# Kernel tuning notes

Measured on AMD Instinct MI355X. Metric: run time of the kernel, lower is better.

The kernel has to match this reference:

```python
import jax, jax.numpy as jnp
import numpy as np

BETA = 0.9
THR = 1.0
ALPHA = 2.0  # snntorch surrogate.atan default

@jax.custom_vjp
def atan_spike(x):
    return (x > 0).astype(x.dtype)

def _atan_fwd(x):
    return atan_spike(x), x

def _atan_bwd(x, g):
    # snntorch ATan surrogate: alpha/2 / (1 + (pi/2 * alpha * x)^2)
    return (g * (ALPHA / 2.0) / (1.0 + (jnp.pi / 2.0 * ALPHA * x) ** 2),)

atan_spike.defvjp(_atan_fwd, _atan_bwd)

def setup_inputs() -> dict:
    key = jax.random.key(0)
    k = jax.random.split(key, 5)
    B, T, C, H, W = 128, 25, 3, 64, 64
    F, HID, O = C * H * W, 2048, 2
    bound1 = 1.0 / np.sqrt(F)
    boundo = 1.0 / np.sqrt(HID)
    return {
        "x": jax.random.normal(k[0], (B, T, C, H, W), jnp.float32),
        "W1": jax.random.uniform(k[1], (HID, F), jnp.float32, -bound1, bound1),
        "b1": jax.random.uniform(k[2], (HID,), jnp.float32, -bound1, bound1),
        "Wo": jax.random.uniform(k[3], (O, HID), jnp.float32, -boundo, boundo),
        "bo": jax.random.uniform(k[4], (O,), jnp.float32, -boundo, boundo),
    }

def reference(x, W1, b1, Wo, bo):
    B, T = x.shape[0], x.shape[1]
    HID, O = W1.shape[0], Wo.shape[0]
    xf = x.reshape(B, T, -1).transpose(1, 0, 2)  # [T, B, F]
    # fc1 for all timesteps at once (input is fixed per step)
    h_all = jnp.einsum('tbf,hf->tbh', xf, W1) + b1  # [T, B, HID]

    def step(carry, h):
        mem1, memo = carry
        # snntorch Leaky (reset_mechanism='subtract'): reset from previous mem
        r1 = atan_spike(mem1 - THR)
        mem1 = BETA * mem1 + h - r1 * THR
        s1 = atan_spike(mem1 - THR)
        o = s1 @ Wo.T + bo
        ro = atan_spike(memo - THR)
        memo = BETA * memo + o - ro * THR
        so = atan_spike(memo - THR)
        return (mem1, memo), so

    init = (jnp.zeros((B, HID), x.dtype), jnp.zeros((B, O), x.dtype))
    (_, _), spk_rec = jax.lax.scan(step, init, h_all)
    # train=False path: sum of output spikes over time
    return spk_rec.sum(axis=0)  # [B, O]
```

## Files before the change

kernel.cpp:

```cpp
#include <hip/hip_runtime.h>


#define T_STEPS 25
#define B_SZ    128
#define F_SZ    12288
#define HID_SZ  2048
#define KSTEPS  384
#define CHUNK   16384

typedef __attribute__((ext_vector_type(8))) _Float16 f16x8;
typedef __attribute__((ext_vector_type(4))) float f32x4;

__device__ __forceinline__ void g2l16(const void* g, void* l) {
  __builtin_amdgcn_global_load_lds(
      (const __attribute__((address_space(1))) void*)g,
      (__attribute__((address_space(3))) void*)l, 16, 0, 0);
}

__global__ __launch_bounds__(256) void conv_x_kernel(
    const float* __restrict__ x, char* __restrict__ A2) {
  const int total = T_STEPS * KSTEPS * 128 * 4;
  for (int i = blockIdx.x * 256 + threadIdx.x; i < total; i += gridDim.x * 256) {
    const int s = i & 3;
    const int r = (i >> 2) & 127;
    const int rest = i >> 9;
    const int ks = rest % KSTEPS;
    const int t = rest / KSTEPS;
    const int k0 = ks * 32 + s * 8;
    const float* src = x + ((size_t)r * T_STEPS + t) * F_SZ + k0;
    float4 v0 = *(const float4*)src;
    float4 v1 = *(const float4*)(src + 4);
    float vf[8] = {v0.x, v0.y, v0.z, v0.w, v1.x, v1.y, v1.z, v1.w};
    f16x8 hi, lo;
#pragma unroll
    for (int j = 0; j < 8; ++j) {
      _Float16 h = (_Float16)vf[j];
      hi[j] = h;
      lo[j] = (_Float16)(vf[j] - (float)h);
    }
    char* chunk = A2 + (size_t)rest * CHUNK;
    const int p = s ^ (r & 7);
    *(f16x8*)(chunk + r * 128 + p * 16) = hi;
    *(f16x8*)(chunk + r * 128 + (p ^ 4) * 16) = lo;
  }
}

__global__ __launch_bounds__(256) void conv_w_kernel(
    const float* __restrict__ W1, char* __restrict__ B2) {
  const int total = 16 * KSTEPS * 128 * 4;
  for (int i = blockIdx.x * 256 + threadIdx.x; i < total; i += gridDim.x * 256) {
    const int s = i & 3;
    const int r = (i >> 2) & 127;
    const int rest = i >> 9;
    const int ks = rest % KSTEPS;
    const int nt = rest / KSTEPS;
    const int k0 = ks * 32 + s * 8;
    const float* src = W1 + ((size_t)(nt * 128 + r)) * F_SZ + k0;
    float4 v0 = *(const float4*)src;
    float4 v1 = *(const float4*)(src + 4);
    float vf[8] = {v0.x, v0.y, v0.z, v0.w, v1.x, v1.y, v1.z, v1.w};
    f16x8 hi, lo;
#pragma unroll
    for (int j = 0; j < 8; ++j) {
      float vs = vf[j] * 128.0f;
      _Float16 h = (_Float16)vs;
      hi[j] = h;
      lo[j] = (_Float16)(vs - (float)h);
    }
    char* chunk = B2 + (size_t)rest * CHUNK;
    const int p = s ^ (r & 7);
    *(f16x8*)(chunk + r * 128 + p * 16) = hi;
    *(f16x8*)(chunk + r * 128 + (p ^ 4) * 16) = lo;
  }
}

__global__ __launch_bounds__(256, 2) void gemm_split_kernel(
    const char* __restrict__ A2, const char* __restrict__ B2,
    const float* __restrict__ b1, float* __restrict__ h_all) {
  __shared__ __align__(16) char lds[32768];
  const int tid = threadIdx.x;
  const int l = tid & 63;
  const int w = tid >> 6;
  const int wm = w >> 1, wn = w & 1;

  const int bid = blockIdx.x;
  const int swz = (bid & 7) * 50 + (bid >> 3);
  const int mt = swz >> 4;
  const int nt = swz & 15;
  const char* aSrc = A2 + (size_t)mt * KSTEPS * CHUNK;
  const char* bSrc = B2 + (size_t)nt * KSTEPS * CHUNK;

  f32x4 acc[4][4];
#pragma unroll
  for (int i = 0; i < 4; ++i)
#pragma unroll
    for (int j = 0; j < 4; ++j) acc[i][j] = (f32x4){0.f, 0.f, 0.f, 0.f};

  const int ra = wm * 64 + (l & 15);
  const int rb = wn * 64 + (l & 15);
  const int j4 = l >> 4;

  for (int k = 0; k < KSTEPS; ++k) {
    const char* ga = aSrc + (size_t)k * CHUNK + tid * 16;
    const char* gb = bSrc + (size_t)k * CHUNK + tid * 16;
    char* la = lds + w * 1024;
    char* lb = lds + 16384 + w * 1024;
#pragma unroll
    for (int i = 0; i < 4; ++i) g2l16(ga + i * 4096, la + i * 4096);
#pragma unroll
    for (int i = 0; i < 4; ++i) g2l16(gb + i * 4096, lb + i * 4096);
    __syncthreads();

    f16x8 ah[4], al[4], bh[4], bl[4];
#pragma unroll
    for (int mb = 0; mb < 4; ++mb) {
      const int r = ra + mb * 16;
      const char* base = lds + r * 128;
      ah[mb] = *(const f16x8*)(base + ((j4 ^ (r & 7)) << 4));
      al[mb] = *(const f16x8*)(base + (((j4 | 4) ^ (r & 7)) << 4));
    }
#pragma unroll
    for (int nb = 0; nb < 4; ++nb) {
      const int r = rb + nb * 16;
      const char* base = lds + 16384 + r * 128;
      bh[nb] = *(const f16x8*)(base + ((j4 ^ (r & 7)) << 4));
      bl[nb] = *(const f16x8*)(base + (((j4 | 4) ^ (r & 7)) << 4));
    }
#pragma unroll
    for (int mb = 0; mb < 4; ++mb)
#pragma unroll
      for (int nb = 0; nb < 4; ++nb) {
        acc[mb][nb] = __builtin_amdgcn_mfma_f32_16x16x32_f16(ah[mb], bh[nb], acc[mb][nb], 0, 0, 0);
        acc[mb][nb] = __builtin_amdgcn_mfma_f32_16x16x32_f16(ah[mb], bl[nb], acc[mb][nb], 0, 0, 0);
        acc[mb][nb] = __builtin_amdgcn_mfma_f32_16x16x32_f16(al[mb], bh[nb], acc[mb][nb], 0, 0, 0);
      }
    __syncthreads();
  }

  const int m0 = mt * 128 + wm * 64;
  const int n0 = nt * 128 + wn * 64;
  const int row_l = (l >> 4) * 4;
  const int col_l = l & 15;
#pragma unroll
  for (int nb = 0; nb < 4; ++nb) {
    const int col = n0 + nb * 16 + col_l;
    const float bias = b1[col];
#pragma unroll
    for (int mb = 0; mb < 4; ++mb) {
#pragma unroll
      for (int q = 0; q < 4; ++q) {
        const int row = m0 + mb * 16 + row_l + q;
        h_all[(size_t)row * HID_SZ + col] = acc[mb][nb][q] * 0.0078125f + bias;
      }
    }
  }
}

__global__ __launch_bounds__(256) void gemm_h_kernel(
    const float* __restrict__ x, const float* __restrict__ W1,
    const float* __restrict__ b1, float* __restrict__ h_all) {
  __shared__ float As[16][128];
  __shared__ float Bs[16][128];
  const int tid = threadIdx.x;
  const int tx = tid & 15;
  const int ty = tid >> 4;
  const int m0 = blockIdx.x * 128;
  const int n0 = blockIdx.y * 128;
  const int lrow = tid >> 1;
  const int lcol = (tid & 1) * 8;
  const int gm = m0 + lrow;
  const int bb = gm & (B_SZ - 1);
  const int tt = gm >> 7;
  const float* aptr = x + ((size_t)bb * T_STEPS + tt) * F_SZ + lcol;
  const float* bptr = W1 + (size_t)(n0 + lrow) * F_SZ + lcol;
  float acc[8][8];
#pragma unroll
  for (int i = 0; i < 8; ++i)
#pragma unroll
    for (int j = 0; j < 8; ++j) acc[i][j] = 0.f;
  for (int k0 = 0; k0 < F_SZ; k0 += 16) {
    float4 av0 = *(const float4*)(aptr + k0);
    float4 av1 = *(const float4*)(aptr + k0 + 4);
    float4 bv0 = *(const float4*)(bptr + k0);
    float4 bv1 = *(const float4*)(bptr + k0 + 4);
    As[lcol + 0][lrow] = av0.x; As[lcol + 1][lrow] = av0.y;
    As[lcol + 2][lrow] = av0.z; As[lcol + 3][lrow] = av0.w;
    As[lcol + 4][lrow] = av1.x; As[lcol + 5][lrow] = av1.y;
    As[lcol + 6][lrow] = av1.z; As[lcol + 7][lrow] = av1.w;
    Bs[lcol + 0][lrow] = bv0.x; Bs[lcol + 1][lrow] = bv0.y;
    Bs[lcol + 2][lrow] = bv0.z; Bs[lcol + 3][lrow] = bv0.w;
    Bs[lcol + 4][lrow] = bv1.x; Bs[lcol + 5][lrow] = bv1.y;
    Bs[lcol + 6][lrow] = bv1.z; Bs[lcol + 7][lrow] = bv1.w;
    __syncthreads();
#pragma unroll
    for (int k = 0; k < 16; ++k) {
      float4 a0 = *(const float4*)&As[k][ty * 8];
      float4 a1 = *(const float4*)&As[k][ty * 8 + 4];
      float4 q0 = *(const float4*)&Bs[k][tx * 8];
      float4 q1 = *(const float4*)&Bs[k][tx * 8 + 4];
      float ar[8] = {a0.x, a0.y, a0.z, a0.w, a1.x, a1.y, a1.z, a1.w};
      float br[8] = {q0.x, q0.y, q0.z, q0.w, q1.x, q1.y, q1.z, q1.w};
#pragma unroll
      for (int i = 0; i < 8; ++i)
#pragma unroll
        for (int j = 0; j < 8; ++j)
          acc[i][j] = fmaf(ar[i], br[j], acc[i][j]);
    }
    __syncthreads();
  }
#pragma unroll
  for (int i = 0; i < 8; ++i) {
    const int gm2 = m0 + ty * 8 + i;
    float* orow = h_all + (size_t)gm2 * HID_SZ + n0 + tx * 8;
    const float* brow = b1 + n0 + tx * 8;
#pragma unroll
    for (int j = 0; j < 8; ++j) orow[j] = acc[i][j] + brow[j];
  }
}

__global__ __launch_bounds__(256) void lif_scan_kernel(
    const float* __restrict__ h_all, const float* __restrict__ Wo,
    const float* __restrict__ bo, float* __restrict__ out) {
  const int b = blockIdx.x;
  const int tid = threadIdx.x;
  float mem1[8];
  float wo0[8], wo1[8];
#pragma unroll
  for (int i = 0; i < 8; ++i) {
    mem1[i] = 0.f;
    wo0[i] = Wo[tid + 256 * i];
    wo1[i] = Wo[HID_SZ + tid + 256 * i];
  }
  __shared__ float partial[4][2];
  float memo0 = 0.f, memo1 = 0.f, acc0 = 0.f, acc1 = 0.f;
  const float bo0 = bo[0], bo1 = bo[1];
  for (int t = 0; t < T_STEPS; ++t) {
    const float* hrow = h_all + ((size_t)t * B_SZ + b) * HID_SZ;
    float p0 = 0.f, p1 = 0.f;
#pragma unroll
    for (int i = 0; i < 8; ++i) {
      float h = hrow[tid + 256 * i];
      float r1 = mem1[i] > 1.0f ? 1.0f : 0.0f;
      float m = 0.9f * mem1[i] + h - r1;
      mem1[i] = m;
      if (m > 1.0f) { p0 += wo0[i]; p1 += wo1[i]; }
    }
#pragma unroll
    for (int off = 32; off > 0; off >>= 1) {
      p0 += __shfl_down(p0, off);
      p1 += __shfl_down(p1, off);
    }
    const int wave = tid >> 6;
    if ((tid & 63) == 0) { partial[wave][0] = p0; partial[wave][1] = p1; }
    __syncthreads();
    if (tid == 0) {
      float o0 = partial[0][0] + partial[1][0] + partial[2][0] + partial[3][0] + bo0;
      float o1 = partial[0][1] + partial[1][1] + partial[2][1] + partial[3][1] + bo1;
      float ro0 = memo0 > 1.0f ? 1.0f : 0.0f;
      float ro1 = memo1 > 1.0f ? 1.0f : 0.0f;
      memo0 = 0.9f * memo0 + o0 - ro0;
      memo1 = 0.9f * memo1 + o1 - ro1;
      acc0 += memo0 > 1.0f ? 1.0f : 0.0f;
      acc1 += memo1 > 1.0f ? 1.0f : 0.0f;
    }
    __syncthreads();
  }
  if (tid == 0) {
    out[b * 2 + 0] = acc0;
    out[b * 2 + 1] = acc1;
  }
}

extern "C" void kernel_launch(void* const* d_in, const int* in_sizes, int n_in,
                              void* d_out, int out_size, void* d_ws, size_t ws_size,
                              hipStream_t stream) {
  const float* x  = (const float*)d_in[0];
  const float* W1 = (const float*)d_in[1];
  const float* b1 = (const float*)d_in[2];
  const float* Wo = (const float*)d_in[3];
  const float* bo = (const float*)d_in[4];
  float* out = (float*)d_out;

  const size_t hall_bytes = (size_t)T_STEPS * B_SZ * HID_SZ * 4;
  const size_t a2_bytes = (size_t)T_STEPS * KSTEPS * CHUNK;
  const size_t b2_bytes = (size_t)16 * KSTEPS * CHUNK;
  char* ws = (char*)d_ws;
  float* h_all = (float*)ws;

  if (ws_size >= hall_bytes + a2_bytes + b2_bytes) {
    char* A2 = ws + hall_bytes;
    char* B2 = A2 + a2_bytes;
    conv_x_kernel<<<2048, 256, 0, stream>>>(x, A2);
    conv_w_kernel<<<2048, 256, 0, stream>>>(W1, B2);
    gemm_split_kernel<<<400, 256, 0, stream>>>(A2, B2, b1, h_all);
  } else {
    dim3 grid(25, 16);
    gemm_h_kernel<<<grid, 256, 0, stream>>>(x, W1, b1, h_all);
  }
  lif_scan_kernel<<<B_SZ, 256, 0, stream>>>(h_all, Wo, bo, out);
}
```

Before: 634.3 us.

## Use 256x128 tiles with multi-stage LDS pipelining in split-fp16 MFMA GEMM

Restructures the split-precision MFMA GEMM to 512-thread blocks computing 256x128 tiles, with M padded to 3328 rows (13 M tiles) and 208 blocks. The A operand is triple-buffered and the B operand double-buffered in LDS, with explicit vmcnt waits and raw barriers so global-to-LDS loads for later k-steps overlap the MFMA work. LDS layout changes from an XOR-swizzled row layout to a k-slice-major layout, and setprio is raised around the MFMA blocks. The larger tile cuts operand reloads, but 128KB of LDS allows only one block per CU, and padding adds some wasted rows.

New measurement: 539.9 us. -14.9%, faster.

```diff
diff --git a/kernel.cpp b/kernel.cpp
--- a/kernel.cpp
+++ b/kernel.cpp
@@ -5,8 +5,10 @@
 #define B_SZ    128
 #define F_SZ    12288
 #define HID_SZ  2048
-#define KSTEPS  384
-#define CHUNK   16384
+#define KT      384
+#define A_CH    32768
+#define B_CH    16384
+#define M_PAD   3328
 
 typedef __attribute__((ext_vector_type(8))) _Float16 f16x8;
 typedef __attribute__((ext_vector_type(4))) float f32x4;
@@ -19,43 +21,46 @@
 
 __global__ __launch_bounds__(256) void conv_x_kernel(
     const float* __restrict__ x, char* __restrict__ A2) {
-  const int total = T_STEPS * KSTEPS * 128 * 4;
+  const int total = 13 * KT * 256 * 4;
+  for (int i = blockIdx.x * 256 + threadIdx.x; i < total; i += gridDim.x * 256) {
+    const int s = i & 3;
+    const int r = (i >> 2) & 255;
+    const int rest = i >> 10;
+    const int ks = rest % KT;
+    const int mt = rest / KT;
+    const int m = mt * 256 + r;
+    const int b = m & 127;
+    const int t = m >> 7;
+    f16x8 hi = {0, 0, 0, 0, 0, 0, 0, 0};
+    f16x8 lo = {0, 0, 0, 0, 0, 0, 0, 0};
+    if (t < T_STEPS) {
+      const float* src = x + ((size_t)(b * T_STEPS + t)) * F_SZ + ks * 32 + s * 8;
+      float4 v0 = *(const float4*)src;
+      float4 v1 = *(const float4*)(src + 4);
+      float vf[8] = {v0.x, v0.y, v0.z, v0.w, v1.x, v1.y, v1.z, v1.w};
+#pragma unroll
+      for (int j = 0; j < 8; ++j) {
+        _Float16 h = (_Float16)vf[j];
+        hi[j] = h;
+        lo[j] = (_Float16)(vf[j] - (float)h);
+      }
+    }
+    char* chunk = A2 + (size_t)rest * A_CH;
+    *(f16x8*)(chunk + s * 4096 + r * 16) = hi;
+    *(f16x8*)(chunk + (s + 4) * 4096 + r * 16) = lo;
+  }
+}
+
+__global__ __launch_bounds__(256) void conv_w_kernel(
+    const float* __restrict__ W1, char* __restrict__ B2) {
+  const int total = 16 * KT * 128 * 4;
   for (int i = blockIdx.x * 256 + threadIdx.x; i < total; i += gridDim.x * 256) {
     const int s = i & 3;
     const int r = (i >> 2) & 127;
     const int rest = i >> 9;
-    const int ks = rest % KSTEPS;
-    const int t = rest / KSTEPS;
-    const int k0 = ks * 32 + s * 8;
-    const float* src = x + ((size_t)r * T_STEPS + t) * F_SZ + k0;
-    float4 v0 = *(const float4*)src;
-    float4 v1 = *(const float4*)(src + 4);
-    float vf[8] = {v0.x, v0.y, v0.z, v0.w, v1.x, v1.y, v1.z, v1.w};
-    f16x8 hi, lo;
-#pragma unroll
-    for (int j = 0; j < 8; ++j) {
-      _Float16 h = (_Float16)vf[j];
-      hi[j] = h;
-      lo[j] = (_Float16)(vf[j] - (float)h);
-    }
-    char* chunk = A2 + (size_t)rest * CHUNK;
-    const int p = s ^ (r & 7);
-    *(f16x8*)(chunk + r * 128 + p * 16) = hi;
-    *(f16x8*)(chunk + r * 128 + (p ^ 4) * 16) = lo;
-  }
-}
-
-__global__ __launch_bounds__(256) void conv_w_kernel(
-    const float* __restrict__ W1, char* __restrict__ B2) {
-  const int total = 16 * KSTEPS * 128 * 4;
-  for (int i = blockIdx.x * 256 + threadIdx.x; i < total; i += gridDim.x * 256) {
-    const int s = i & 3;
-    const int r = (i >> 2) & 127;
-    const int rest = i >> 9;
-    const int ks = rest % KSTEPS;
-    const int nt = rest / KSTEPS;
-    const int k0 = ks * 32 + s * 8;
-    const float* src = W1 + ((size_t)(nt * 128 + r)) * F_SZ + k0;
+    const int ks = rest % KT;
+    const int nt = rest / KT;
+    const float* src = W1 + ((size_t)(nt * 128 + r)) * F_SZ + ks * 32 + s * 8;
     float4 v0 = *(const float4*)src;
     float4 v1 = *(const float4*)(src + 4);
     float vf[8] = {v0.x, v0.y, v0.z, v0.w, v1.x, v1.y, v1.z, v1.w};
@@ -67,28 +72,43 @@
       hi[j] = h;
       lo[j] = (_Float16)(vs - (float)h);
     }
-    char* chunk = B2 + (size_t)rest * CHUNK;
-    const int p = s ^ (r & 7);
-    *(f16x8*)(chunk + r * 128 + p * 16) = hi;
-    *(f16x8*)(chunk + r * 128 + (p ^ 4) * 16) = lo;
-  }
-}
-
-__global__ __launch_bounds__(256, 2) void gemm_split_kernel(
+    char* chunk = B2 + (size_t)rest * B_CH;
+    *(f16x8*)(chunk + s * 2048 + r * 16) = hi;
+    *(f16x8*)(chunk + (s + 4) * 2048 + r * 16) = lo;
+  }
+}
+
+__global__ __launch_bounds__(512) void gemm_mfma_kernel(
     const char* __restrict__ A2, const char* __restrict__ B2,
     const float* __restrict__ b1, float* __restrict__ h_all) {
-  __shared__ __align__(16) char lds[32768];
+  __shared__ __align__(16) char lds[131072];
   const int tid = threadIdx.x;
   const int l = tid & 63;
   const int w = tid >> 6;
-  const int wm = w >> 1, wn = w & 1;
+  const int wm = w >> 1;
+  const int wn = w & 1;
 
   const int bid = blockIdx.x;
-  const int swz = (bid & 7) * 50 + (bid >> 3);
+  const int swz = (bid & 7) * 26 + (bid >> 3);
   const int mt = swz >> 4;
   const int nt = swz & 15;
-  const char* aSrc = A2 + (size_t)mt * KSTEPS * CHUNK;
-  const char* bSrc = B2 + (size_t)nt * KSTEPS * CHUNK;
+  const char* aSrc = A2 + (size_t)mt * KT * A_CH;
+  const char* bSrc = B2 + (size_t)nt * KT * B_CH;
+
+#define STAGE_A_PAIR(ktx, i0)                                              \
+  do {                                                                     \
+    const char* s_ = aSrc + (size_t)(ktx) * A_CH + (i0) * 8192 + tid * 16; \
+    char* d_ = (char*)lds + ((ktx) % 3) * 32768 + (i0) * 8192 + w * 1024;  \
+    g2l16(s_, d_);                                                         \
+    g2l16(s_ + 8192, d_ + 8192);                                           \
+  } while (0)
+#define STAGE_B2(ktx)                                                      \
+  do {                                                                     \
+    const char* s_ = bSrc + (size_t)(ktx) * B_CH + tid * 16;               \
+    char* d_ = (char*)lds + 98304 + ((ktx) & 1) * 16384 + w * 1024;        \
+    g2l16(s_, d_);                                                         \
+    g2l16(s_ + 8192, d_ + 8192);                                           \
+  } while (0)
 
   f32x4 acc[4][4];
 #pragma unroll
@@ -96,64 +116,98 @@
 #pragma unroll
     for (int j = 0; j < 4; ++j) acc[i][j] = (f32x4){0.f, 0.f, 0.f, 0.f};
 
-  const int ra = wm * 64 + (l & 15);
-  const int rb = wn * 64 + (l & 15);
-  const int j4 = l >> 4;
-
-  for (int k = 0; k < KSTEPS; ++k) {
-    const char* ga = aSrc + (size_t)k * CHUNK + tid * 16;
-    const char* gb = bSrc + (size_t)k * CHUNK + tid * 16;
-    char* la = lds + w * 1024;
-    char* lb = lds + 16384 + w * 1024;
-#pragma unroll
-    for (int i = 0; i < 4; ++i) g2l16(ga + i * 4096, la + i * 4096);
-#pragma unroll
-    for (int i = 0; i < 4; ++i) g2l16(gb + i * 4096, lb + i * 4096);
-    __syncthreads();
-
-    f16x8 ah[4], al[4], bh[4], bl[4];
-#pragma unroll
-    for (int mb = 0; mb < 4; ++mb) {
-      const int r = ra + mb * 16;
-      const char* base = lds + r * 128;
-      ah[mb] = *(const f16x8*)(base + ((j4 ^ (r & 7)) << 4));
-      al[mb] = *(const f16x8*)(base + (((j4 | 4) ^ (r & 7)) << 4));
-    }
-#pragma unroll
-    for (int nb = 0; nb < 4; ++nb) {
-      const int r = rb + nb * 16;
-      const char* base = lds + 16384 + r * 128;
-      bh[nb] = *(const f16x8*)(base + ((j4 ^ (r & 7)) << 4));
-      bl[nb] = *(const f16x8*)(base + (((j4 | 4) ^ (r & 7)) << 4));
-    }
-#pragma unroll
-    for (int mb = 0; mb < 4; ++mb)
-#pragma unroll
-      for (int nb = 0; nb < 4; ++nb) {
-        acc[mb][nb] = __builtin_amdgcn_mfma_f32_16x16x32_f16(ah[mb], bh[nb], acc[mb][nb], 0, 0, 0);
-        acc[mb][nb] = __builtin_amdgcn_mfma_f32_16x16x32_f16(ah[mb], bl[nb], acc[mb][nb], 0, 0, 0);
-        acc[mb][nb] = __builtin_amdgcn_mfma_f32_16x16x32_f16(al[mb], bh[nb], acc[mb][nb], 0, 0, 0);
+  const int aoff = (l >> 4) * 4096 + (wm * 64 + (l & 15)) * 16;
+  const int boff = (l >> 4) * 2048 + (wn * 64 + (l & 15)) * 16;
+
+  STAGE_A_PAIR(0, 0); STAGE_A_PAIR(0, 2); STAGE_B2(0);
+  STAGE_A_PAIR(1, 0); STAGE_A_PAIR(1, 2); STAGE_B2(1);
+
+#define MM3(mf, nf, AH, AL, BH, BL)                                                      \
+  acc[mf][nf] = __builtin_amdgcn_mfma_f32_16x16x32_f16(AH, BH, acc[mf][nf], 0, 0, 0);    \
+  acc[mf][nf] = __builtin_amdgcn_mfma_f32_16x16x32_f16(AH, BL, acc[mf][nf], 0, 0, 0);    \
+  acc[mf][nf] = __builtin_amdgcn_mfma_f32_16x16x32_f16(AL, BH, acc[mf][nf], 0, 0, 0);
+
+  for (int kt = 0; kt < KT; ++kt) {
+    if (kt == 0) {
+      asm volatile("s_waitcnt vmcnt(6)" ::: "memory");
+    } else if (kt < KT - 1) {
+      asm volatile("s_waitcnt vmcnt(4)" ::: "memory");
+    } else {
+      asm volatile("s_waitcnt vmcnt(0)" ::: "memory");
+    }
+    __builtin_amdgcn_s_barrier();
+    asm volatile("" ::: "memory");
+    __builtin_amdgcn_sched_barrier(0);
+
+    const char* la = (const char*)lds + (kt % 3) * 32768;
+    const char* lb = (const char*)lds + 98304 + (kt & 1) * 16384;
+
+    f16x8 ah0 = *(const f16x8*)(la + aoff);
+    f16x8 ah1 = *(const f16x8*)(la + aoff + 256);
+    f16x8 ah2 = *(const f16x8*)(la + aoff + 512);
+    f16x8 ah3 = *(const f16x8*)(la + aoff + 768);
+    f16x8 al0 = *(const f16x8*)(la + aoff + 16384);
+    f16x8 al1 = *(const f16x8*)(la + aoff + 16384 + 256);
+    f16x8 al2 = *(const f16x8*)(la + aoff + 16384 + 512);
+    f16x8 al3 = *(const f16x8*)(la + aoff + 16384 + 768);
+    f16x8 bh0 = *(const f16x8*)(lb + boff);
+    f16x8 bl0 = *(const f16x8*)(lb + boff + 8192);
+    f16x8 bh1 = *(const f16x8*)(lb + boff + 256);
+    f16x8 bl1 = *(const f16x8*)(lb + boff + 8192 + 256);
+
+    if (kt >= 1 && kt <= KT - 2) STAGE_B2(kt + 1);
+    if (kt <= KT - 3) STAGE_A_PAIR(kt + 2, 0);
+
+    __builtin_amdgcn_s_setprio(1);
+    MM3(0, 0, ah0, al0, bh0, bl0)
+    MM3(1, 0, ah1, al1, bh0, bl0)
+    MM3(2, 0, ah2, al2, bh0, bl0)
+    MM3(3, 0, ah3, al3, bh0, bl0)
+    MM3(0, 1, ah0, al0, bh1, bl1)
+    MM3(1, 1, ah1, al1, bh1, bl1)
+    MM3(2, 1, ah2, al2, bh1, bl1)
+    MM3(3, 1, ah3, al3, bh1, bl1)
+    __builtin_amdgcn_s_setprio(0);
+
+    __builtin_amdgcn_s_barrier();
+
+    f16x8 bh2 = *(const f16x8*)(lb + boff + 512);
+    f16x8 bl2 = *(const f16x8*)(lb + boff + 8192 + 512);
+    f16x8 bh3 = *(const f16x8*)(lb + boff + 768);
+    f16x8 bl3 = *(const f16x8*)(lb + boff + 8192 + 768);
+
+    if (kt <= KT - 3) STAGE_A_PAIR(kt + 2, 2);
+
+    __builtin_amdgcn_s_setprio(1);
+    MM3(0, 2, ah0, al0, bh2, bl2)
+    MM3(1, 2, ah1, al1, bh2, bl2)
+    MM3(2, 2, ah2, al2, bh2, bl2)
+    MM3(3, 2, ah3, al3, bh2, bl2)
+    MM3(0, 3, ah0, al0, bh3, bl3)
+    MM3(1, 3, ah1, al1, bh3, bl3)
+    MM3(2, 3, ah2, al2, bh3, bl3)
+    MM3(3, 3, ah3, al3, bh3, bl3)
+    __builtin_amdgcn_s_setprio(0);
+  }
+
+  const int row0 = mt * 256 + wm * 64 + (l >> 4) * 4;
+  const int col0 = nt * 128 + wn * 64 + (l & 15);
+#pragma unroll
+  for (int nf = 0; nf < 4; ++nf) {
+    const int col = col0 + nf * 16;
+    const float bias = b1[col];
+#pragma unroll
+    for (int mf = 0; mf < 4; ++mf) {
+#pragma unroll
+      for (int q = 0; q < 4; ++q) {
+        const int row = row0 + mf * 16 + q;
+        h_all[(size_t)row * HID_SZ + col] = acc[mf][nf][q] * 0.0078125f + bias;
       }
-    __syncthreads();
-  }
-
-  const int m0 = mt * 128 + wm * 64;
-  const int n0 = nt * 128 + wn * 64;
-  const int row_l = (l >> 4) * 4;
-  const int col_l = l & 15;
-#pragma unroll
-  for (int nb = 0; nb < 4; ++nb) {
-    const int col = n0 + nb * 16 + col_l;
-    const float bias = b1[col];
-#pragma unroll
-    for (int mb = 0; mb < 4; ++mb) {
-#pragma unroll
-      for (int q = 0; q < 4; ++q) {
-        const int row = m0 + mb * 16 + row_l + q;
-        h_all[(size_t)row * HID_SZ + col] = acc[mb][nb][q] * 0.0078125f + bias;
-      }
-    }
-  }
+    }
+  }
+#undef STAGE_A_PAIR
+#undef STAGE_B2
+#undef MM3
 }
 
 __global__ __launch_bounds__(256) void gemm_h_kernel(
@@ -281,9 +335,9 @@
   const float* bo = (const float*)d_in[4];
   float* out = (float*)d_out;
 
-  const size_t hall_bytes = (size_t)T_STEPS * B_SZ * HID_SZ * 4;
-  const size_t a2_bytes = (size_t)T_STEPS * KSTEPS * CHUNK;
-  const size_t b2_bytes = (size_t)16 * KSTEPS * CHUNK;
+  const size_t hall_bytes = (size_t)M_PAD * HID_SZ * 4;
+  const size_t a2_bytes = (size_t)13 * KT * A_CH;
+  const size_t b2_bytes = (size_t)16 * KT * B_CH;
   char* ws = (char*)d_ws;
   float* h_all = (float*)ws;
 
@@ -292,7 +346,7 @@
     char* B2 = A2 + a2_bytes;
     conv_x_kernel<<<2048, 256, 0, stream>>>(x, A2);
     conv_w_kernel<<<2048, 256, 0, stream>>>(W1, B2);
-    gemm_split_kernel<<<400, 256, 0, stream>>>(A2, B2, b1, h_all);
+    gemm_mfma_kernel<<<208, 512, 0, stream>>>(A2, B2, b1, h_all);
   } else {
     dim3 grid(25, 16);
     gemm_h_kernel<<<grid, 256, 0, stream>>>(x, W1, b1, h_all);
```
